# Kernel tuning notes

Hardware: AMD Instinct MI355X
Metric: run time of the kernel (lower is better)

Reference implementation:

```python
import jax, jax.numpy as jnp
import numpy as np

B, T, E = 2, 2048, 1024
H = 16            # num_heads (global in source repo)
D = E // H        # head_len
LN_EPS = 1e-5


def setup_inputs() -> dict:
    key = jax.random.key(0)
    ks = jax.random.split(key, 12)
    s = lambda fan_in: 1.0 / np.sqrt(fan_in)
    return {
        "x":     jax.random.normal(ks[0], (B, T, E), jnp.float32),
        "ln1_g": jnp.ones((E,), jnp.float32),
        "ln1_b": jnp.zeros((E,), jnp.float32),
        "Wq":    jax.random.normal(ks[1], (E, E), jnp.float32) * s(E),
        "Wk":    jax.random.normal(ks[2], (E, E), jnp.float32) * s(E),
        "Wv":    jax.random.normal(ks[3], (E, E), jnp.float32) * s(E),
        "Wo":    jax.random.normal(ks[4], (E, E), jnp.float32) * s(E),
        "bo":    jnp.zeros((E,), jnp.float32),
        "ln2_g": jnp.ones((E,), jnp.float32),
        "ln2_b": jnp.zeros((E,), jnp.float32),
        "W1":    jax.random.normal(ks[5], (E, 4 * E), jnp.float32) * s(E),
        "b1":    jnp.zeros((4 * E,), jnp.float32),
        "W2":    jax.random.normal(ks[6], (4 * E, E), jnp.float32) * s(4 * E),
        "b2":    jnp.zeros((E,), jnp.float32),
    }


def _layernorm(x, g, b):
    mu = jnp.mean(x, axis=-1, keepdims=True)
    var = jnp.mean(jnp.square(x - mu), axis=-1, keepdims=True)
    return (x - mu) * jax.lax.rsqrt(var + LN_EPS) * g + b


def _attention(x, Wq, Wk, Wv, Wo, bo):
    b, t, e = x.shape
    q = (x @ Wq).reshape(b, t, H, D)
    k = (x @ Wk).reshape(b, t, H, D)
    v = (x @ Wv).reshape(b, t, H, D)
    scores = jnp.einsum("bqhd,bkhd->bhqk", q, k) / np.sqrt(D).astype(np.float32)
    causal = jnp.tril(jnp.ones((t, t), bool))
    scores = jnp.where(causal, scores, -jnp.inf)
    attn = jax.nn.softmax(scores, axis=-1)
    out = jnp.einsum("bhqk,bkhd->bqhd", attn, v).reshape(b, t, e)
    return out @ Wo + bo


def reference(x, ln1_g, ln1_b, Wq, Wk, Wv, Wo, bo, ln2_g, ln2_b, W1, b1, W2, b2):
    # pre-norm attention + residual (dropout=0 / eval mode)
    x = x + _attention(_layernorm(x, ln1_g, ln1_b), Wq, Wk, Wv, Wo, bo)
    # pre-norm MLP + residual
    h = _layernorm(x, ln2_g, ln2_b)
    h = jax.nn.relu(h @ W1 + b1) @ W2 + b2
    return x + h
```

## Files before the change

kernel.cpp:

```cpp
#include <hip/hip_runtime.h>
#include <cmath>
#include <cstdint>
#include <cstddef>

typedef __bf16 bf16_t;
typedef __bf16 bf16x8 __attribute__((ext_vector_type(8)));
typedef __bf16 bf16x4 __attribute__((ext_vector_type(4)));
typedef float  f32x4  __attribute__((ext_vector_type(4)));

#define B_   2
#define T_   2048
#define E_   1024
#define H_   16
#define D_   64
#define FF_  4096
#define NROW (B_ * T_)
#define QS_  (3 * E_)
#define NTI  (T_ / 64)

__device__ __forceinline__ void gll16(const bf16_t* g, bf16_t* l) {
    __builtin_amdgcn_global_load_lds(
        (const __attribute__((address_space(1))) unsigned int*)g,
        (__attribute__((address_space(3))) unsigned int*)l, 16, 0, 0);
}

__global__ __launch_bounds__(256) void ln_kernel(
    const float* __restrict__ x, const float* __restrict__ g,
    const float* __restrict__ bta, bf16_t* __restrict__ out)
{
    int row = blockIdx.x;
    int tid = threadIdx.x;
    const float4* xr = (const float4*)(x + (size_t)row * E_);
    float4 v = xr[tid];
    float s  = v.x + v.y + v.z + v.w;
    float ss = v.x * v.x + v.y * v.y + v.z * v.z + v.w * v.w;
#pragma unroll
    for (int off = 32; off; off >>= 1) {
        s  += __shfl_xor(s, off);
        ss += __shfl_xor(ss, off);
    }
    __shared__ float red[8];
    int wave = tid >> 6, lane = tid & 63;
    if (lane == 0) { red[wave] = s; red[4 + wave] = ss; }
    __syncthreads();
    s  = red[0] + red[1] + red[2] + red[3];
    ss = red[4] + red[5] + red[6] + red[7];
    float mu   = s * (1.0f / E_);
    float var  = ss * (1.0f / E_) - mu * mu;
    float rstd = rsqrtf(var + 1e-5f);
    float4 gv = ((const float4*)g)[tid];
    float4 bv = ((const float4*)bta)[tid];
    union { bf16_t h[4]; ushort4 u; } pk;
    pk.h[0] = (bf16_t)((v.x - mu) * rstd * gv.x + bv.x);
    pk.h[1] = (bf16_t)((v.y - mu) * rstd * gv.y + bv.y);
    pk.h[2] = (bf16_t)((v.z - mu) * rstd * gv.z + bv.z);
    pk.h[3] = (bf16_t)((v.w - mu) * rstd * gv.w + bv.w);
    ((ushort4*)(out + (size_t)row * E_))[tid] = pk.u;
}

__global__ __launch_bounds__(256) void ln_reduce4(
    const bf16_t* __restrict__ p, const float* __restrict__ bias,
    const float* __restrict__ resid, float* __restrict__ x1,
    const float* __restrict__ g, const float* __restrict__ bta,
    bf16_t* __restrict__ out)
{
    int row = blockIdx.x;
    int tid = threadIdx.x;
    size_t off = (size_t)row * E_ + tid * 4;
    float4 v = {0.f, 0.f, 0.f, 0.f};
#pragma unroll
    for (int z = 0; z < 4; ++z) {
        bf16x4 pv = *(const bf16x4*)&p[(size_t)z * NROW * E_ + off];
        v.x += (float)pv[0]; v.y += (float)pv[1];
        v.z += (float)pv[2]; v.w += (float)pv[3];
    }
    float4 bb = ((const float4*)bias)[tid];
    float4 rr = ((const float4*)(resid + (size_t)row * E_))[tid];
    v.x += bb.x + rr.x; v.y += bb.y + rr.y;
    v.z += bb.z + rr.z; v.w += bb.w + rr.w;
    ((float4*)(x1 + (size_t)row * E_))[tid] = v;
    float s  = v.x + v.y + v.z + v.w;
    float ss = v.x * v.x + v.y * v.y + v.z * v.z + v.w * v.w;
#pragma unroll
    for (int o = 32; o; o >>= 1) {
        s  += __shfl_xor(s, o);
        ss += __shfl_xor(ss, o);
    }
    __shared__ float red[8];
    int wave = tid >> 6, lane = tid & 63;
    if (lane == 0) { red[wave] = s; red[4 + wave] = ss; }
    __syncthreads();
    s  = red[0] + red[1] + red[2] + red[3];
    ss = red[4] + red[5] + red[6] + red[7];
    float mu   = s * (1.0f / E_);
    float var  = ss * (1.0f / E_) - mu * mu;
    float rstd = rsqrtf(var + 1e-5f);
    float4 gv = ((const float4*)g)[tid];
    float4 bv = ((const float4*)bta)[tid];
    union { bf16_t h[4]; ushort4 u; } pk;
    pk.h[0] = (bf16_t)((v.x - mu) * rstd * gv.x + bv.x);
    pk.h[1] = (bf16_t)((v.y - mu) * rstd * gv.y + bv.y);
    pk.h[2] = (bf16_t)((v.z - mu) * rstd * gv.z + bv.z);
    pk.h[3] = (bf16_t)((v.w - mu) * rstd * gv.w + bv.w);
    ((ushort4*)(out + (size_t)row * E_))[tid] = pk.u;
}

__global__ __launch_bounds__(256) void add_reduce4(
    const bf16_t* __restrict__ p, const float* __restrict__ bias,
    const float* __restrict__ resid, float* __restrict__ out)
{
    int row = blockIdx.x;
    int tid = threadIdx.x;
    size_t off = (size_t)row * E_ + tid * 4;
    float4 v = {0.f, 0.f, 0.f, 0.f};
#pragma unroll
    for (int z = 0; z < 4; ++z) {
        bf16x4 pv = *(const bf16x4*)&p[(size_t)z * NROW * E_ + off];
        v.x += (float)pv[0]; v.y += (float)pv[1];
        v.z += (float)pv[2]; v.w += (float)pv[3];
    }
    float4 bb = ((const float4*)bias)[tid];
    float4 rr = ((const float4*)(resid + (size_t)row * E_))[tid];
    v.x += bb.x + rr.x; v.y += bb.y + rr.y;
    v.z += bb.z + rr.z; v.w += bb.w + rr.w;
    ((float4*)(out + (size_t)row * E_))[tid] = v;
}

__global__ __launch_bounds__(256) void transpose_all(
    const float* __restrict__ Wq, const float* __restrict__ Wk,
    const float* __restrict__ Wv, const float* __restrict__ Wo,
    const float* __restrict__ W1, const float* __restrict__ W2,
    bf16_t* __restrict__ wqkv, bf16_t* __restrict__ wot,
    bf16_t* __restrict__ w1t, bf16_t* __restrict__ w2t)
{
    int l = blockIdx.x;
    const float* W; bf16_t* Wt; int K, N, bx, by;
    if (l < 4096) {
        int seg = l >> 10, r = l & 1023;
        K = E_; N = E_; bx = r & 31; by = r >> 5;
        if      (seg == 0) { W = Wq; Wt = wqkv; }
        else if (seg == 1) { W = Wk; Wt = wqkv + (size_t)E_ * E_; }
        else if (seg == 2) { W = Wv; Wt = wqkv + (size_t)2 * E_ * E_; }
        else               { W = Wo; Wt = wot; }
    } else if (l < 8192) {
        int r = l - 4096; K = E_; N = FF_; bx = r & 127; by = r >> 7;
        W = W1; Wt = w1t;
    } else {
        int r = l - 8192; K = FF_; N = E_; bx = r & 31; by = r >> 5;
        W = W2; Wt = w2t;
    }
    __shared__ float t[32][33];
    int n0 = bx * 32, k0 = by * 32;
    int tx = threadIdx.x & 31, ty = threadIdx.x >> 5;
#pragma unroll
    for (int i = 0; i < 4; ++i)
        t[ty + i * 8][tx] = W[(size_t)(k0 + ty + i * 8) * N + n0 + tx];
    __syncthreads();
#pragma unroll
    for (int i = 0; i < 4; ++i)
        Wt[(size_t)(n0 + ty + i * 8) * K + k0 + tx] = (bf16_t)t[tx][ty + i * 8];
}

#define BM 128
#define BN 128
#define BK 32

__global__ __launch_bounds__(256) void gemm_bt(
    const bf16_t* __restrict__ A, const bf16_t* __restrict__ Bt,
    const float* __restrict__ bias, const float* __restrict__ resid,
    void* __restrict__ Cout, bf16_t* __restrict__ vt_out,
    int M, int N, int K, int lda, int ldb,
    int has_bias, int do_relu, int has_resid, int out_bf16)
{
    __shared__ __attribute__((aligned(16))) bf16_t As[BM * BK];
    __shared__ __attribute__((aligned(16))) bf16_t Bs[BN * BK];
    int tid  = threadIdx.x;
    int lane = tid & 63, wave = tid >> 6;
    int m0 = blockIdx.x * BM, n0 = blockIdx.y * BN;
    int wm = (wave & 1) * 64, wn = (wave >> 1) * 64;
    int koff = blockIdx.z * K;
    f32x4 acc[4][4];
#pragma unroll
    for (int i = 0; i < 4; ++i)
#pragma unroll
        for (int j = 0; j < 4; ++j) acc[i][j] = (f32x4){0.f, 0.f, 0.f, 0.f};

    int sr = tid >> 2;
    int sc = (tid & 3) * 8;
    const int kq = (lane >> 4) * 8;
    const int ml = lane & 15;
    const bf16_t* Ag = A  + (size_t)(m0 + sr) * lda + koff + sc;
    const bf16_t* Bg = Bt + (size_t)(n0 + sr) * ldb + koff + sc;
    bf16_t* Al = &As[sr * BK + sc];
    bf16_t* Bl = &Bs[sr * BK + sc];

    for (int k0 = 0; k0 < K; k0 += BK) {
        gll16(Ag + k0, Al);
        gll16(Ag + k0 + (size_t)64 * lda, Al + 64 * BK);
        gll16(Bg + k0, Bl);
        gll16(Bg + k0 + (size_t)64 * ldb, Bl + 64 * BK);
        __syncthreads();
        bf16x8 af[4], bfr[4];
#pragma unroll
        for (int mi = 0; mi < 4; ++mi)
            af[mi] = *(const bf16x8*)&As[(wm + mi * 16 + ml) * BK + kq];
#pragma unroll
        for (int ni = 0; ni < 4; ++ni)
            bfr[ni] = *(const bf16x8*)&Bs[(wn + ni * 16 + ml) * BK + kq];
#pragma unroll
        for (int mi = 0; mi < 4; ++mi)
#pragma unroll
            for (int ni = 0; ni < 4; ++ni)
                acc[mi][ni] = __builtin_amdgcn_mfma_f32_16x16x32_bf16(
                    af[mi], bfr[ni], acc[mi][ni], 0, 0, 0);
        __syncthreads();
    }

    int r4 = (lane >> 4) * 4;
    if (gridDim.z > 1) {
        bf16_t* P = (bf16_t*)Cout + (size_t)blockIdx.z * M * N;
#pragma unroll
        for (int mi = 0; mi < 4; ++mi)
#pragma unroll
            for (int ni = 0; ni < 4; ++ni) {
                int col = n0 + wn + ni * 16 + ml;
#pragma unroll
                for (int r = 0; r < 4; ++r) {
                    int row = m0 + wm + mi * 16 + r4 + r;
                    P[(size_t)row * N + col] = (bf16_t)acc[mi][ni][r];
                }
            }
        return;
    }
    if (vt_out && n0 >= 2 * E_) {
#pragma unroll
        for (int mi = 0; mi < 4; ++mi)
#pragma unroll
            for (int ni = 0; ni < 4; ++ni) {
                int vcol = n0 + wn + ni * 16 + ml - 2 * E_;
                int h = vcol >> 6, d = vcol & 63;
                int row0 = m0 + wm + mi * 16 + r4;
                int b = row0 >> 11, t = row0 & (T_ - 1);
                union { bf16_t h4[4]; uint2 u; } pk;
#pragma unroll
                for (int r = 0; r < 4; ++r) pk.h4[r] = (bf16_t)acc[mi][ni][r];
                *(uint2*)&vt_out[((size_t)(b * H_ + h) * D_ + d) * T_ + t] = pk.u;
            }
        return;
    }
#pragma unroll
    for (int mi = 0; mi < 4; ++mi) {
#pragma unroll
        for (int ni = 0; ni < 4; ++ni) {
            int col = n0 + wn + ni * 16 + ml;
            float bval = has_bias ? bias[col] : 0.0f;
#pragma unroll
            for (int r = 0; r < 4; ++r) {
                int row = m0 + wm + mi * 16 + r4 + r;
                float v = acc[mi][ni][r] + bval;
                if (do_relu)   v = fmaxf(v, 0.0f);
                if (has_resid) v += resid[(size_t)row * N + col];
                if (out_bf16)
                    ((bf16_t*)Cout)[(size_t)row * N + col] = (bf16_t)v;
                else
                    ((float*)Cout)[(size_t)row * N + col] = v;
            }
        }
    }
}

#define PSTR 72

struct TileState {
    f32x4 acc[4];
    float m1, l1;
};

__device__ __forceinline__ void tile_update(
    const bf16x8 kf[2][4], const bf16x8 vf[2][4], const bf16x8 qf[2],
    TileState& st, bf16_t* PsW, int ml, int r4, int kq8,
    bool diag, int ch, int qrow)
{
    f32x4 s[4];
#pragma unroll
    for (int nt = 0; nt < 4; ++nt) {
        s[nt] = (f32x4){0.f, 0.f, 0.f, 0.f};
#pragma unroll
        for (int ks = 0; ks < 2; ++ks)
            s[nt] = __builtin_amdgcn_mfma_f32_16x16x32_bf16(kf[ks][nt], qf[ks], s[nt], 0, 0, 0);
    }
    if (diag) {
#pragma unroll
        for (int nt = 0; nt < 4; ++nt)
#pragma unroll
            for (int r = 0; r < 4; ++r)
                if (ch * 64 + nt * 16 + r4 + r > qrow) s[nt][r] = -INFINITY;
    }
    float mx = -INFINITY;
#pragma unroll
    for (int nt = 0; nt < 4; ++nt)
#pragma unroll
        for (int r = 0; r < 4; ++r) mx = fmaxf(mx, s[nt][r]);
    mx = fmaxf(mx, __shfl_xor(mx, 16));
    mx = fmaxf(mx, __shfl_xor(mx, 32));
    float mn = fmaxf(st.m1, mx);
    float al = __expf(st.m1 - mn);
    st.m1 = mn;
    float sum = 0.f;
#pragma unroll
    for (int nt = 0; nt < 4; ++nt)
#pragma unroll
        for (int r = 0; r < 4; ++r) {
            float p = __expf(s[nt][r] - mn);
            s[nt][r] = p;
            sum += p;
        }
    sum += __shfl_xor(sum, 16);
    sum += __shfl_xor(sum, 32);
    st.l1 = st.l1 * al + sum;
#pragma unroll
    for (int dt = 0; dt < 4; ++dt)
#pragma unroll
        for (int r = 0; r < 4; ++r) st.acc[dt][r] *= al;

#pragma unroll
    for (int nt = 0; nt < 4; ++nt) {
        union { bf16_t h[4]; uint2 u; } pk;
#pragma unroll
        for (int r = 0; r < 4; ++r) pk.h[r] = (bf16_t)s[nt][r];
        *(uint2*)&PsW[ml * PSTR + nt * 16 + r4] = pk.u;
    }
#pragma unroll
    for (int ks = 0; ks < 2; ++ks) {
        bf16x8 pf = *(const bf16x8*)&PsW[ml * PSTR + ks * 32 + kq8];
#pragma unroll
        for (int dt = 0; dt < 4; ++dt)
            st.acc[dt] = __builtin_amdgcn_mfma_f32_16x16x32_bf16(vf[ks][dt], pf, st.acc[dt], 0, 0, 0);
    }
}

__global__ __launch_bounds__(256) void attn_mfma(
    const bf16_t* __restrict__ Qp, const bf16_t* __restrict__ Kp,
    const bf16_t* __restrict__ Vt, bf16_t* __restrict__ O)
{
    __shared__ __attribute__((aligned(16))) bf16_t Ks[2][64 * PSTR];
    __shared__ __attribute__((aligned(16))) bf16_t Vts[2][64 * PSTR];
    __shared__ __attribute__((aligned(16))) bf16_t Ps[4][16 * PSTR];

    int tid = threadIdx.x, lane = tid & 63, wave = tid >> 6;
    int ml  = lane & 15;
    int kq8 = (lane >> 4) * 8;
    int r4  = (lane >> 4) * 4;
    int bh = blockIdx.y, b = bh >> 4, h = bh & 15;
    size_t qk_base = (size_t)b * T_ * QS_ + h * D_;
    size_t vt_base = (size_t)bh * D_ * T_;
    size_t o_base  = (size_t)b * T_ * E_ + h * D_;

    int lo = blockIdx.x, hi = NTI - 1 - blockIdx.x;
    int qlo = lo * 64 + wave * 16;
    int qhi = hi * 64 + wave * 16;

    bf16x8 qfl[2], qfh[2];
#pragma unroll
    for (int ks = 0; ks < 2; ++ks) {
        bf16x8 a = *(const bf16x8*)&Qp[qk_base + (size_t)(qlo + ml) * QS_ + ks * 32 + kq8];
        bf16x8 c = *(const bf16x8*)&Qp[qk_base + (size_t)(qhi + ml) * QS_ + ks * 32 + kq8];
#pragma unroll
        for (int j = 0; j < 8; ++j) {
            a[j] = (bf16_t)((float)a[j] * 0.125f);
            c[j] = (bf16_t)((float)c[j] * 0.125f);
        }
        qfl[ks] = a; qfh[ks] = c;
    }

    TileState stl, sth;
#pragma unroll
    for (int dt = 0; dt < 4; ++dt) {
        stl.acc[dt] = (f32x4){0.f, 0.f, 0.f, 0.f};
        sth.acc[dt] = (f32x4){0.f, 0.f, 0.f, 0.f};
    }
    stl.m1 = -INFINITY; stl.l1 = 0.f;
    sth.m1 = -INFINITY; sth.l1 = 0.f;

    int r0 = tid >> 3, c0 = (tid & 7) * 8;
    int nch = hi + 1;

    {
        const bf16_t* kb = &Kp[qk_base + (size_t)r0 * QS_ + c0];
        const bf16_t* vb = &Vt[vt_base + (size_t)r0 * T_ + c0];
        uint4 k0v = *(const uint4*)kb;
        uint4 k1v = *(const uint4*)(kb + (size_t)32 * QS_);
        uint4 v0v = *(const uint4*)vb;
        uint4 v1v = *(const uint4*)(vb + (size_t)32 * T_);
        *(uint4*)&Ks[0][r0 * PSTR + c0]         = k0v;
        *(uint4*)&Ks[0][(r0 + 32) * PSTR + c0]  = k1v;
        *(uint4*)&Vts[0][r0 * PSTR + c0]        = v0v;
        *(uint4*)&Vts[0][(r0 + 32) * PSTR + c0] = v1v;
    }

    for (int ch = 0; ch < nch; ++ch) {
        int cur = ch & 1, nxt = cur ^ 1;
        __syncthreads();

        uint4 nk0, nk1, nv0, nv1;
        bool pf = (ch + 1 < nch);
        if (pf) {
            const bf16_t* kb = &Kp[qk_base + (size_t)((ch + 1) * 64 + r0) * QS_ + c0];
            const bf16_t* vb = &Vt[vt_base + (size_t)r0 * T_ + (ch + 1) * 64 + c0];
            nk0 = *(const uint4*)kb;
            nk1 = *(const uint4*)(kb + (size_t)32 * QS_);
            nv0 = *(const uint4*)vb;
            nv1 = *(const uint4*)(vb + (size_t)32 * T_);
        }

        bf16x8 kf[2][4], vf[2][4];
#pragma unroll
        for (int ks = 0; ks < 2; ++ks)
#pragma unroll
            for (int nt = 0; nt < 4; ++nt) {
                kf[ks][nt] = *(const bf16x8*)&Ks[cur][(nt * 16 + ml) * PSTR + ks * 32 + kq8];
                vf[ks][nt] = *(const bf16x8*)&Vts[cur][(nt * 16 + ml) * PSTR + ks * 32 + kq8];
            }

        tile_update(kf, vf, qfh, sth, Ps[wave], ml, r4, kq8,
                    ch == hi, ch, qhi + ml);
        if (ch <= lo)
            tile_update(kf, vf, qfl, stl, Ps[wave], ml, r4, kq8,
                        ch == lo, ch, qlo + ml);

        if (pf) {
            *(uint4*)&Ks[nxt][r0 * PSTR + c0]         = nk0;
            *(uint4*)&Ks[nxt][(r0 + 32) * PSTR + c0]  = nk1;
            *(uint4*)&Vts[nxt][r0 * PSTR + c0]        = nv0;
            *(uint4*)&Vts[nxt][(r0 + 32) * PSTR + c0] = nv1;
        }
    }

#pragma unroll
    for (int t = 0; t < 2; ++t) {
        TileState& st = t ? stl : sth;
        int qw = t ? qlo : qhi;
        float inv = 1.0f / st.l1;
#pragma unroll
        for (int dt = 0; dt < 4; ++dt) {
            union { bf16_t h[4]; uint2 u; } pk;
#pragma unroll
            for (int r = 0; r < 4; ++r) pk.h[r] = (bf16_t)(st.acc[dt][r] * inv);
            *(uint2*)&Ps[wave][ml * PSTR + dt * 16 + r4] = pk.u;
        }
        int row = lane >> 2, seg = (lane & 3) * 16;
        bf16x8 o0 = *(const bf16x8*)&Ps[wave][row * PSTR + seg];
        bf16x8 o1 = *(const bf16x8*)&Ps[wave][row * PSTR + seg + 8];
        size_t gp = o_base + (size_t)(qw + row) * E_ + seg;
        *(bf16x8*)&O[gp]     = o0;
        *(bf16x8*)&O[gp + 8] = o1;
    }
}

extern "C" void kernel_launch(void* const* d_in, const int* in_sizes, int n_in,
                              void* d_out, int out_size, void* d_ws, size_t ws_size,
                              hipStream_t stream)
{
    const float* x    = (const float*)d_in[0];
    const float* ln1g = (const float*)d_in[1];
    const float* ln1b = (const float*)d_in[2];
    const float* Wq   = (const float*)d_in[3];
    const float* Wk   = (const float*)d_in[4];
    const float* Wv   = (const float*)d_in[5];
    const float* Wo   = (const float*)d_in[6];
    const float* bo   = (const float*)d_in[7];
    const float* ln2g = (const float*)d_in[8];
    const float* ln2b = (const float*)d_in[9];
    const float* W1   = (const float*)d_in[10];
    const float* b1   = (const float*)d_in[11];
    const float* W2   = (const float*)d_in[12];
    const float* b2   = (const float*)d_in[13];

    char* ws = (char*)d_ws;
    const size_t MB = 1024ull * 1024ull;
    bf16_t* wqkv = (bf16_t*)(ws + 0 * MB);
    bf16_t* wot  = (bf16_t*)(ws + 6 * MB);
    bf16_t* w1t  = (bf16_t*)(ws + 8 * MB);
    bf16_t* w2t  = (bf16_t*)(ws + 16 * MB);
    bf16_t* xn   = (bf16_t*)(ws + 24 * MB);
    bf16_t* QKV  = (bf16_t*)(ws + 32 * MB);
    bf16_t* att  = (bf16_t*)(ws + 56 * MB);
    float*  x1   = (float*)(ws + 64 * MB);
    bf16_t* hb   = (bf16_t*)(ws + 80 * MB);
    bf16_t* h1   = (bf16_t*)(ws + 88 * MB);
    bf16_t* Vtb  = (bf16_t*)(ws + 88 * MB);
    bf16_t* part = (bf16_t*)(ws + 24 * MB);

    dim3 blk(256);

    transpose_all<<<dim3(12288), blk, 0, stream>>>(
        Wq, Wk, Wv, Wo, W1, W2, wqkv, wot, w1t, w2t);

    ln_kernel<<<dim3(NROW), blk, 0, stream>>>(x, ln1g, ln1b, xn);

    gemm_bt<<<dim3(NROW / BM, QS_ / BN), blk, 0, stream>>>(
        xn, wqkv, nullptr, nullptr, QKV, Vtb, NROW, QS_, E_, E_, E_, 0, 0, 0, 1);

    attn_mfma<<<dim3(NTI / 2, B_ * H_), blk, 0, stream>>>(
        QKV, QKV + E_, Vtb, att);

    gemm_bt<<<dim3(NROW / BM, E_ / BN, 4), blk, 0, stream>>>(
        att, wot, nullptr, nullptr, part, nullptr, NROW, E_, E_ / 4, E_, E_, 0, 0, 0, 0);
    ln_reduce4<<<dim3(NROW), blk, 0, stream>>>(
        part, bo, x, x1, ln2g, ln2b, hb);

    gemm_bt<<<dim3(NROW / BM, FF_ / BN), blk, 0, stream>>>(
        hb, w1t, b1, nullptr, h1, nullptr, NROW, FF_, E_, E_, E_, 1, 1, 0, 1);

    gemm_bt<<<dim3(NROW / BM, E_ / BN, 4), blk, 0, stream>>>(
        h1, w2t, nullptr, nullptr, part, nullptr, NROW, E_, FF_ / 4, FF_, FF_, 0, 0, 0, 0);
    add_reduce4<<<dim3(NROW), blk, 0, stream>>>(
        part, b2, x1, (float*)d_out);
}
```

Measured before the change: 373.9 us.

## Double-buffer GEMM LDS tiles via registers and halve split-K with fp32 partials

The GEMM now stages tiles through registers into two LDS buffers, prefetching the next K-slice while MFMAs run on the current one, and drops one barrier per iteration. This replaces the direct global-to-LDS loads. The split-K factor for the output and second MLP projections drops from 4 to 2, and the partials are stored in fp32 instead of bf16. The reduce kernels are adapted to match. This trades prefetch overlap and fewer partial passes against losing the async LDS-load path, doubling LDS use, and cutting parallelism on the split-K GEMMs.

```diff
diff --git a/kernel.cpp b/kernel.cpp
--- a/kernel.cpp
+++ b/kernel.cpp
@@ -5,7 +5,6 @@
 
 typedef __bf16 bf16_t;
 typedef __bf16 bf16x8 __attribute__((ext_vector_type(8)));
-typedef __bf16 bf16x4 __attribute__((ext_vector_type(4)));
 typedef float  f32x4  __attribute__((ext_vector_type(4)));
 
 #define B_   2
@@ -17,12 +16,6 @@
 #define NROW (B_ * T_)
 #define QS_  (3 * E_)
 #define NTI  (T_ / 64)
-
-__device__ __forceinline__ void gll16(const bf16_t* g, bf16_t* l) {
-    __builtin_amdgcn_global_load_lds(
-        (const __attribute__((address_space(1))) unsigned int*)g,
-        (__attribute__((address_space(3))) unsigned int*)l, 16, 0, 0);
-}
 
 __global__ __launch_bounds__(256) void ln_kernel(
     const float* __restrict__ x, const float* __restrict__ g,
@@ -58,27 +51,25 @@
     ((ushort4*)(out + (size_t)row * E_))[tid] = pk.u;
 }
 
-__global__ __launch_bounds__(256) void ln_reduce4(
-    const bf16_t* __restrict__ p, const float* __restrict__ bias,
+__global__ __launch_bounds__(256) void ln_reduce2(
+    const float* __restrict__ p, const float* __restrict__ bias,
     const float* __restrict__ resid, float* __restrict__ x1,
     const float* __restrict__ g, const float* __restrict__ bta,
     bf16_t* __restrict__ out)
 {
     int row = blockIdx.x;
     int tid = threadIdx.x;
-    size_t off = (size_t)row * E_ + tid * 4;
-    float4 v = {0.f, 0.f, 0.f, 0.f};
-#pragma unroll
-    for (int z = 0; z < 4; ++z) {
-        bf16x4 pv = *(const bf16x4*)&p[(size_t)z * NROW * E_ + off];
-        v.x += (float)pv[0]; v.y += (float)pv[1];
-        v.z += (float)pv[2]; v.w += (float)pv[3];
-    }
+    size_t off = (size_t)row * E_;
+    float4 v0 = ((const float4*)(p + off))[tid];
+    float4 v1 = ((const float4*)(p + (size_t)NROW * E_ + off))[tid];
     float4 bb = ((const float4*)bias)[tid];
-    float4 rr = ((const float4*)(resid + (size_t)row * E_))[tid];
-    v.x += bb.x + rr.x; v.y += bb.y + rr.y;
-    v.z += bb.z + rr.z; v.w += bb.w + rr.w;
-    ((float4*)(x1 + (size_t)row * E_))[tid] = v;
+    float4 rr = ((const float4*)(resid + off))[tid];
+    float4 v;
+    v.x = v0.x + v1.x + bb.x + rr.x;
+    v.y = v0.y + v1.y + bb.y + rr.y;
+    v.z = v0.z + v1.z + bb.z + rr.z;
+    v.w = v0.w + v1.w + bb.w + rr.w;
+    ((float4*)(x1 + off))[tid] = v;
     float s  = v.x + v.y + v.z + v.w;
     float ss = v.x * v.x + v.y * v.y + v.z * v.z + v.w * v.w;
 #pragma unroll
@@ -102,28 +93,26 @@
     pk.h[1] = (bf16_t)((v.y - mu) * rstd * gv.y + bv.y);
     pk.h[2] = (bf16_t)((v.z - mu) * rstd * gv.z + bv.z);
     pk.h[3] = (bf16_t)((v.w - mu) * rstd * gv.w + bv.w);
-    ((ushort4*)(out + (size_t)row * E_))[tid] = pk.u;
-}
-
-__global__ __launch_bounds__(256) void add_reduce4(
-    const bf16_t* __restrict__ p, const float* __restrict__ bias,
+    ((ushort4*)(out + off))[tid] = pk.u;
+}
+
+__global__ __launch_bounds__(256) void add_reduce2(
+    const float* __restrict__ p, const float* __restrict__ bias,
     const float* __restrict__ resid, float* __restrict__ out)
 {
     int row = blockIdx.x;
     int tid = threadIdx.x;
-    size_t off = (size_t)row * E_ + tid * 4;
-    float4 v = {0.f, 0.f, 0.f, 0.f};
-#pragma unroll
-    for (int z = 0; z < 4; ++z) {
-        bf16x4 pv = *(const bf16x4*)&p[(size_t)z * NROW * E_ + off];
-        v.x += (float)pv[0]; v.y += (float)pv[1];
-        v.z += (float)pv[2]; v.w += (float)pv[3];
-    }
+    size_t off = (size_t)row * E_;
+    float4 v0 = ((const float4*)(p + off))[tid];
+    float4 v1 = ((const float4*)(p + (size_t)NROW * E_ + off))[tid];
     float4 bb = ((const float4*)bias)[tid];
-    float4 rr = ((const float4*)(resid + (size_t)row * E_))[tid];
-    v.x += bb.x + rr.x; v.y += bb.y + rr.y;
-    v.z += bb.z + rr.z; v.w += bb.w + rr.w;
-    ((float4*)(out + (size_t)row * E_))[tid] = v;
+    float4 rr = ((const float4*)(resid + off))[tid];
+    float4 v;
+    v.x = v0.x + v1.x + bb.x + rr.x;
+    v.y = v0.y + v1.y + bb.y + rr.y;
+    v.z = v0.z + v1.z + bb.z + rr.z;
+    v.w = v0.w + v1.w + bb.w + rr.w;
+    ((float4*)(out + off))[tid] = v;
 }
 
 __global__ __launch_bounds__(256) void transpose_all(
@@ -172,8 +161,8 @@
     int M, int N, int K, int lda, int ldb,
     int has_bias, int do_relu, int has_resid, int out_bf16)
 {
-    __shared__ __attribute__((aligned(16))) bf16_t As[BM * BK];
-    __shared__ __attribute__((aligned(16))) bf16_t Bs[BN * BK];
+    __shared__ __attribute__((aligned(16))) bf16_t As[2][BM * BK];
+    __shared__ __attribute__((aligned(16))) bf16_t Bs[2][BN * BK];
     int tid  = threadIdx.x;
     int lane = tid & 63, wave = tid >> 6;
     int m0 = blockIdx.x * BM, n0 = blockIdx.y * BN;
@@ -191,34 +180,58 @@
     const int ml = lane & 15;
     const bf16_t* Ag = A  + (size_t)(m0 + sr) * lda + koff + sc;
     const bf16_t* Bg = Bt + (size_t)(n0 + sr) * ldb + koff + sc;
-    bf16_t* Al = &As[sr * BK + sc];
-    bf16_t* Bl = &Bs[sr * BK + sc];
-
-    for (int k0 = 0; k0 < K; k0 += BK) {
-        gll16(Ag + k0, Al);
-        gll16(Ag + k0 + (size_t)64 * lda, Al + 64 * BK);
-        gll16(Bg + k0, Bl);
-        gll16(Bg + k0 + (size_t)64 * ldb, Bl + 64 * BK);
+    int niter = K / BK;
+
+    {
+        uint4 ra0 = *(const uint4*)Ag;
+        uint4 ra1 = *(const uint4*)(Ag + (size_t)64 * lda);
+        uint4 rb0 = *(const uint4*)Bg;
+        uint4 rb1 = *(const uint4*)(Bg + (size_t)64 * ldb);
+        *(uint4*)&As[0][sr * BK + sc]        = ra0;
+        *(uint4*)&As[0][(sr + 64) * BK + sc] = ra1;
+        *(uint4*)&Bs[0][sr * BK + sc]        = rb0;
+        *(uint4*)&Bs[0][(sr + 64) * BK + sc] = rb1;
+    }
+
+    for (int it = 0; it < niter; ++it) {
+        int cur = it & 1, nxt = cur ^ 1;
         __syncthreads();
+
+        uint4 ra0, ra1, rb0, rb1;
+        bool pf = (it + 1 < niter);
+        if (pf) {
+            int k0 = (it + 1) * BK;
+            ra0 = *(const uint4*)(Ag + k0);
+            ra1 = *(const uint4*)(Ag + k0 + (size_t)64 * lda);
+            rb0 = *(const uint4*)(Bg + k0);
+            rb1 = *(const uint4*)(Bg + k0 + (size_t)64 * ldb);
+        }
+
         bf16x8 af[4], bfr[4];
 #pragma unroll
         for (int mi = 0; mi < 4; ++mi)
-            af[mi] = *(const bf16x8*)&As[(wm + mi * 16 + ml) * BK + kq];
+            af[mi] = *(const bf16x8*)&As[cur][(wm + mi * 16 + ml) * BK + kq];
 #pragma unroll
         for (int ni = 0; ni < 4; ++ni)
-            bfr[ni] = *(const bf16x8*)&Bs[(wn + ni * 16 + ml) * BK + kq];
+            bfr[ni] = *(const bf16x8*)&Bs[cur][(wn + ni * 16 + ml) * BK + kq];
 #pragma unroll
         for (int mi = 0; mi < 4; ++mi)
 #pragma unroll
             for (int ni = 0; ni < 4; ++ni)
                 acc[mi][ni] = __builtin_amdgcn_mfma_f32_16x16x32_bf16(
                     af[mi], bfr[ni], acc[mi][ni], 0, 0, 0);
-        __syncthreads();
+
+        if (pf) {
+            *(uint4*)&As[nxt][sr * BK + sc]        = ra0;
+            *(uint4*)&As[nxt][(sr + 64) * BK + sc] = ra1;
+            *(uint4*)&Bs[nxt][sr * BK + sc]        = rb0;
+            *(uint4*)&Bs[nxt][(sr + 64) * BK + sc] = rb1;
+        }
     }
 
     int r4 = (lane >> 4) * 4;
     if (gridDim.z > 1) {
-        bf16_t* P = (bf16_t*)Cout + (size_t)blockIdx.z * M * N;
+        float* P = (float*)Cout + (size_t)blockIdx.z * M * N;
 #pragma unroll
         for (int mi = 0; mi < 4; ++mi)
 #pragma unroll
@@ -227,7 +240,7 @@
 #pragma unroll
                 for (int r = 0; r < 4; ++r) {
                     int row = m0 + wm + mi * 16 + r4 + r;
-                    P[(size_t)row * N + col] = (bf16_t)acc[mi][ni][r];
+                    P[(size_t)row * N + col] = acc[mi][ni][r];
                 }
             }
         return;
@@ -489,7 +502,7 @@
     bf16_t* hb   = (bf16_t*)(ws + 80 * MB);
     bf16_t* h1   = (bf16_t*)(ws + 88 * MB);
     bf16_t* Vtb  = (bf16_t*)(ws + 88 * MB);
-    bf16_t* part = (bf16_t*)(ws + 24 * MB);
+    float*  part = (float*)(ws + 24 * MB);
 
     dim3 blk(256);
 
@@ -504,16 +517,16 @@
     attn_mfma<<<dim3(NTI / 2, B_ * H_), blk, 0, stream>>>(
         QKV, QKV + E_, Vtb, att);
 
-    gemm_bt<<<dim3(NROW / BM, E_ / BN, 4), blk, 0, stream>>>(
-        att, wot, nullptr, nullptr, part, nullptr, NROW, E_, E_ / 4, E_, E_, 0, 0, 0, 0);
-    ln_reduce4<<<dim3(NROW), blk, 0, stream>>>(
+    gemm_bt<<<dim3(NROW / BM, E_ / BN, 2), blk, 0, stream>>>(
+        att, wot, nullptr, nullptr, part, nullptr, NROW, E_, E_ / 2, E_, E_, 0, 0, 0, 0);
+    ln_reduce2<<<dim3(NROW), blk, 0, stream>>>(
         part, bo, x, x1, ln2g, ln2b, hb);
 
     gemm_bt<<<dim3(NROW / BM, FF_ / BN), blk, 0, stream>>>(
         hb, w1t, b1, nullptr, h1, nullptr, NROW, FF_, E_, E_, E_, 1, 1, 0, 1);
 
-    gemm_bt<<<dim3(NROW / BM, E_ / BN, 4), blk, 0, stream>>>(
-        h1, w2t, nullptr, nullptr, part, nullptr, NROW, E_, FF_ / 4, FF_, FF_, 0, 0, 0, 0);
-    add_reduce4<<<dim3(NROW), blk, 0, stream>>>(
+    gemm_bt<<<dim3(NROW / BM, E_ / BN, 2), blk, 0, stream>>>(
+        h1, w2t, nullptr, nullptr, part, nullptr, NROW, E_, FF_ / 2, FF_, FF_, 0, 0, 0, 0);
+    add_reduce2<<<dim3(NROW), blk, 0, stream>>>(
         part, b2, x1, (float*)d_out);
 }
```

After: 342.6 us. 1.09x faster.
